# Kernel tuning notes

Hardware: AMD Instinct MI355X
Metric: run time of the kernel (lower is better)

The kernel has to match this reference:

```python
import jax, jax.numpy as jnp
import numpy as np
import math

EPS = 1.1920929e-07  # torch.finfo(float32).eps, used by nn.RMSNorm(eps=None)

def rmsnorm(x, w):
    return x * jax.lax.rsqrt(jnp.mean(x * x, axis=-1, keepdims=True) + EPS) * w

def sinkhorn(logits, iters=20):
    m = jnp.exp(logits - logits.max(axis=-1, keepdims=True))
    def body(_, m):
        m = m / (m.sum(axis=-1, keepdims=True) + 1e-6)
        return m / (m.sum(axis=-2, keepdims=True) + 1e-6)
    return jax.lax.fori_loop(0, iters, body, m)

def ngram_hash(ids, mults):
    # ids [B,T] int32, mults [2,2,3] int32 -> [B,T,4]
    B, T = ids.shape
    padded = jnp.pad(ids, ((0, 0), (2, 0)))
    windows = jnp.stack([padded[:, k:k + T] for k in range(3)], axis=-1)  # [B,T,3]
    out = []
    for n_idx in range(2):
        L = n_idx + 2
        grams = windows[:, :, 3 - L:]                                     # [B,T,L]
        mixed = grams[:, :, None, :] * mults[n_idx, :, :L][None, None]    # [B,T,2,L]
        h = mixed[..., 0]
        for k in range(1, L):
            h = jnp.bitwise_xor(h, mixed[..., k])
        out.append(h % 4096)
    return jnp.concatenate(out, axis=2)

def short_conv(x, conv_w, norm_w):
    # depthwise causal conv, kernel 4: torch pads 3 both sides then slices [..., :T]
    B, T, G, C = x.shape
    xn = rmsnorm(x, norm_w).reshape(B, T, G * C).transpose(0, 2, 1)  # [B,GC,T]
    y = jax.lax.conv_general_dilated(xn, conv_w, (1,), [(3, 0)],
                                     feature_group_count=G * C,
                                     dimension_numbers=('NCH', 'OIH', 'NCH'))
    return jax.nn.silu(y).transpose(0, 2, 1).reshape(B, T, G, C)

def engram(x, ids, mults, emb_table, val_w, val_b, key_w, key_b, nq_w, nk_w, conv_w, convnorm_w):
    B, T = ids.shape
    hash_ids = ngram_hash(ids, mults) + jnp.array([0, 4096, 8192, 12288], dtype=jnp.int32)
    emb = emb_table[hash_ids].reshape(B, T, -1)                       # [B,T,256]
    v_base = emb @ val_w + val_b                                      # [B,T,128]
    k = rmsnorm(jnp.einsum('btd,sdc->btsc', emb, key_w) + key_b, nk_w)  # [B,T,4,128]
    q = rmsnorm(x, nq_w)
    gates = jax.nn.sigmoid(jnp.sum(q * k, axis=-1, keepdims=True) / math.sqrt(128.0))
    v_gated = v_base[:, :, None, :] * gates                           # [B,T,4,128]
    return v_gated + short_conv(v_gated, conv_w, convnorm_w)

def causal_attn(x, qkv_w, qkv_b, proj_w, proj_b):
    B, T, C = x.shape
    H, D = 4, C // 4
    q, k, v = jnp.split(x @ qkv_w + qkv_b, 3, axis=-1)
    q = q.reshape(B, T, H, D).transpose(0, 2, 1, 3)
    k = k.reshape(B, T, H, D).transpose(0, 2, 1, 3)
    v = v.reshape(B, T, H, D).transpose(0, 2, 1, 3)
    att = jnp.einsum('bhtd,bhsd->bhts', q, k) / math.sqrt(D)
    att = jnp.where(jnp.tril(jnp.ones((T, T), bool)), att, -jnp.inf)
    att = jax.nn.softmax(att, axis=-1)
    y = jnp.einsum('bhts,bhsd->bhtd', att, v).transpose(0, 2, 1, 3).reshape(B, T, C)
    return y @ proj_w + proj_b

def mhc(x, layer_fn, coef_w, pre_w, pre_b, post_w, post_b, res_w, res_b, a_pre, a_post, a_res, ln_w):
    B, T, n, C = x.shape
    xn = rmsnorm(x.reshape(B * T, n * C), coef_w)
    H_pre = jax.nn.sigmoid(a_pre * (xn @ pre_w + pre_b))             # [BT,n]
    H_post = 2.0 * jax.nn.sigmoid(a_post * (xn @ post_w + post_b))   # [BT,n]
    H_res = sinkhorn((a_res * (xn @ res_w + res_b)).reshape(-1, n, n))
    xp = x.reshape(B * T, n, C)
    x_agg = jnp.einsum('bn,bnc->bc', H_pre, xp)
    y = layer_fn(rmsnorm(x_agg.reshape(B, T, C), ln_w)).reshape(B * T, C)
    # faithful to torch einsum 'bjn,bc->bnc' applied to H_post.transpose(1,2) [BT,n,1]:
    # the stream dim j is CONTRACTED, leaving a size-1 dim that broadcasts over streams
    x_branch = H_post.sum(axis=-1)[:, None, None] * y[:, None, :]    # [BT,1,C]
    x_highway = jnp.einsum('bnm,bmc->bnc', H_res, xp)                # [BT,n,C]
    return (x_highway + x_branch).reshape(B, T, n, C)

def _forward(x, input_ids, eng_multipliers, eng_embedding, eng_val_w, eng_val_b, eng_key_w, eng_key_b, eng_nq_w, eng_nk_w, eng_conv_w, eng_convnorm_w, a_coef_w, a_pre_w, a_pre_b, a_post_w, a_post_b, a_res_w, a_res_b, a_alpha_pre, a_alpha_post, a_alpha_res, a_ln_w, qkv_w, qkv_b, attnproj_w, attnproj_b, m_coef_w, m_pre_w, m_pre_b, m_post_w, m_post_b, m_res_w, m_res_b, m_alpha_pre, m_alpha_post, m_alpha_res, m_ln_w, mlp_w1, mlp_b1, mlp_w2, mlp_b2):
    x = x + engram(x, input_ids, eng_multipliers, eng_embedding, eng_val_w, eng_val_b, eng_key_w, eng_key_b, eng_nq_w, eng_nk_w, eng_conv_w, eng_convnorm_w)
    attn_fn = lambda z: causal_attn(z, qkv_w, qkv_b, attnproj_w, attnproj_b)
    x = mhc(x, attn_fn, a_coef_w, a_pre_w, a_pre_b, a_post_w, a_post_b, a_res_w, a_res_b, a_alpha_pre, a_alpha_post, a_alpha_res, a_ln_w)
    mlp_fn = lambda z: jax.nn.silu(z @ mlp_w1 + mlp_b1) @ mlp_w2 + mlp_b2
    x = mhc(x, mlp_fn, m_coef_w, m_pre_w, m_pre_b, m_post_w, m_post_b, m_res_w, m_res_b, m_alpha_pre, m_alpha_post, m_alpha_res, m_ln_w)
    return x

def setup_inputs():
    key = jax.random.key(0)
    B, T = 256, 128
    def rnd(i, shp, scale=0.02):
        return jax.random.normal(jax.random.fold_in(key, i), shp, jnp.float32) * scale
    alpha = jnp.asarray(0.01, jnp.float32)
    return {
        'x': rnd(0, (B, T, 4, 128), 1.0),
        'input_ids': jax.random.randint(jax.random.fold_in(key, 1), (B, T), 0, 4096, jnp.int32),
        'eng_multipliers': jax.random.randint(jax.random.fold_in(key, 2), (2, 2, 3), 1, 10000, jnp.int32),
        'eng_embedding': rnd(3, (16384, 64)),
        'eng_val_w': rnd(4, (256, 128)), 'eng_val_b': jnp.zeros(128, jnp.float32),
        'eng_key_w': rnd(5, (4, 256, 128)), 'eng_key_b': jnp.zeros((4, 128), jnp.float32),
        'eng_nq_w': jnp.ones((4, 128), jnp.float32), 'eng_nk_w': jnp.ones((4, 128), jnp.float32),
        'eng_conv_w': rnd(6, (512, 1, 4), 0.1), 'eng_convnorm_w': jnp.ones((4, 128), jnp.float32),
        'a_coef_w': jnp.ones(512, jnp.float32),
        'a_pre_w': rnd(7, (512, 4)), 'a_pre_b': jnp.zeros(4, jnp.float32),
        'a_post_w': rnd(8, (512, 4)), 'a_post_b': jnp.zeros(4, jnp.float32),
        'a_res_w': rnd(9, (512, 16)), 'a_res_b': jnp.zeros(16, jnp.float32),
        'a_alpha_pre': alpha, 'a_alpha_post': alpha, 'a_alpha_res': alpha,
        'a_ln_w': jnp.ones(128, jnp.float32),
        'qkv_w': rnd(10, (128, 384)), 'qkv_b': jnp.zeros(384, jnp.float32),
        'attnproj_w': rnd(11, (128, 128)), 'attnproj_b': jnp.zeros(128, jnp.float32),
        'm_coef_w': jnp.ones(512, jnp.float32),
        'm_pre_w': rnd(12, (512, 4)), 'm_pre_b': jnp.zeros(4, jnp.float32),
        'm_post_w': rnd(13, (512, 4)), 'm_post_b': jnp.zeros(4, jnp.float32),
        'm_res_w': rnd(14, (512, 16)), 'm_res_b': jnp.zeros(16, jnp.float32),
        'm_alpha_pre': alpha, 'm_alpha_post': alpha, 'm_alpha_res': alpha,
        'm_ln_w': jnp.ones(128, jnp.float32),
        'mlp_w1': rnd(15, (128, 512)), 'mlp_b1': jnp.zeros(512, jnp.float32),
        'mlp_w2': rnd(16, (512, 128)), 'mlp_b2': jnp.zeros(128, jnp.float32),
    }

def reference(x, input_ids, eng_multipliers, eng_embedding, eng_val_w, eng_val_b, eng_key_w, eng_key_b, eng_nq_w, eng_nk_w, eng_conv_w, eng_convnorm_w, a_coef_w, a_pre_w, a_pre_b, a_post_w, a_post_b, a_res_w, a_res_b, a_alpha_pre, a_alpha_post, a_alpha_res, a_ln_w, qkv_w, qkv_b, attnproj_w, attnproj_b, m_coef_w, m_pre_w, m_pre_b, m_post_w, m_post_b, m_res_w, m_res_b, m_alpha_pre, m_alpha_post, m_alpha_res, m_ln_w, mlp_w1, mlp_b1, mlp_w2, mlp_b2):
    return _forward(x, input_ids, eng_multipliers, eng_embedding, eng_val_w, eng_val_b, eng_key_w, eng_key_b, eng_nq_w, eng_nk_w, eng_conv_w, eng_convnorm_w, a_coef_w, a_pre_w, a_pre_b, a_post_w, a_post_b, a_res_w, a_res_b, a_alpha_pre, a_alpha_post, a_alpha_res, a_ln_w, qkv_w, qkv_b, attnproj_w, attnproj_b, m_coef_w, m_pre_w, m_pre_b, m_post_w, m_post_b, m_res_w, m_res_b, m_alpha_pre, m_alpha_post, m_alpha_res, m_ln_w, mlp_w1, mlp_b1, mlp_w2, mlp_b2)
```

## Files before the change

### kernel.cpp

```cpp
#include <hip/hip_runtime.h>

#define BT 32768
#define TSEQ 128

constexpr float EPSF = 1.1920929e-07f;

typedef __attribute__((ext_vector_type(8))) short bf16x8;
typedef __attribute__((ext_vector_type(4))) float f32x4;

__device__ __forceinline__ float sigm(float z) { return 1.f / (1.f + __expf(-z)); }

__device__ __forceinline__ short bf16c(float f) {
  union { float f; unsigned u; } v; v.f = f;
  unsigned r = v.u + 0x7FFFu + ((v.u >> 16) & 1u);
  return (short)(r >> 16);
}
__device__ __forceinline__ float bf2f(short s) {
  union { unsigned u; float f; } v; v.u = ((unsigned)(unsigned short)s) << 16;
  return v.f;
}

__device__ __forceinline__ float red64(float v) {
  v += __shfl_xor(v, 1);  v += __shfl_xor(v, 2);  v += __shfl_xor(v, 4);
  v += __shfl_xor(v, 8);  v += __shfl_xor(v, 16); v += __shfl_xor(v, 32);
  return v;
}
__device__ __forceinline__ float red32(float v) {
  v += __shfl_xor(v, 1); v += __shfl_xor(v, 2); v += __shfl_xor(v, 4);
  v += __shfl_xor(v, 8); v += __shfl_xor(v, 16);
  return v;
}
__device__ __forceinline__ float red16(float v) {
  v += __shfl_xor(v, 1); v += __shfl_xor(v, 2); v += __shfl_xor(v, 4); v += __shfl_xor(v, 8);
  return v;
}
__device__ __forceinline__ float redmax16(float v) {
  v = fmaxf(v, __shfl_xor(v, 1)); v = fmaxf(v, __shfl_xor(v, 2));
  v = fmaxf(v, __shfl_xor(v, 4)); v = fmaxf(v, __shfl_xor(v, 8));
  return v;
}
__device__ __forceinline__ void load8(float* d, const float* p) {
  const float4 a = *reinterpret_cast<const float4*>(p);
  const float4 b = *reinterpret_cast<const float4*>(p + 4);
  d[0]=a.x; d[1]=a.y; d[2]=a.z; d[3]=a.w; d[4]=b.x; d[5]=b.y; d[6]=b.z; d[7]=b.w;
}

__global__ __launch_bounds__(256) void prep(
    const float* __restrict__ qkv_w, const float* __restrict__ proj_w,
    const float* __restrict__ mlp_w1, const float* __restrict__ mlp_w2,
    const float* __restrict__ val_w, const float* __restrict__ key_w,
    const float* __restrict__ a_res_w, const float* __restrict__ a_pre_w,
    const float* __restrict__ a_post_w,
    const float* __restrict__ m_res_w, const float* __restrict__ m_pre_w,
    const float* __restrict__ m_post_w,
    const float* __restrict__ a_res_b, const float* __restrict__ a_pre_b,
    const float* __restrict__ a_post_b,
    const float* __restrict__ m_res_b, const float* __restrict__ m_pre_b,
    const float* __restrict__ m_post_b,
    short* __restrict__ wt_qkv, short* __restrict__ wt_proj,
    short* __restrict__ wt_mlp1, short* __restrict__ wt_mlp2,
    short* __restrict__ wt_eng, short* __restrict__ wpk_a,
    short* __restrict__ wpk_m, float* __restrict__ bpk_a,
    float* __restrict__ bpk_m)
{
  const int idx = blockIdx.x * 256 + threadIdx.x;
  if (idx < 49152) {
    const int n = idx >> 7, k = idx & 127;
    wt_qkv[idx] = bf16c(qkv_w[k * 384 + n]);
  } else if (idx < 65536) {
    const int j = idx - 49152; const int n = j >> 7, k = j & 127;
    wt_proj[j] = bf16c(proj_w[k * 128 + n]);
  } else if (idx < 131072) {
    const int j = idx - 65536; const int n = j >> 7, k = j & 127;
    wt_mlp1[j] = bf16c(mlp_w1[k * 512 + n]);
  } else if (idx < 196608) {
    const int j = idx - 131072; const int n = j >> 9, k = j & 511;
    wt_mlp2[j] = bf16c(mlp_w2[k * 128 + n]);
  } else if (idx < 360448) {
    const int j = idx - 196608; const int n = j >> 8, k = j & 255;
    float v;
    if (n < 128) v = val_w[k * 128 + n];
    else v = key_w[(size_t)((n - 128) >> 7) * 32768 + k * 128 + (n & 127)];
    wt_eng[j] = bf16c(v);
  } else if (idx < 376832) {
    const int j = idx - 360448; const int r = j >> 9, k = j & 511;
    float v = 0.f;
    if (r < 16) v = a_res_w[k * 16 + r];
    else if (r < 20) v = a_pre_w[k * 4 + (r - 16)];
    else if (r < 24) v = a_post_w[k * 4 + (r - 20)];
    wpk_a[j] = bf16c(v);
  } else if (idx < 393216) {
    const int j = idx - 376832; const int r = j >> 9, k = j & 511;
    float v = 0.f;
    if (r < 16) v = m_res_w[k * 16 + r];
    else if (r < 20) v = m_pre_w[k * 4 + (r - 16)];
    else if (r < 24) v = m_post_w[k * 4 + (r - 20)];
    wpk_m[j] = bf16c(v);
  } else if (idx < 393280) {
    const int j = idx - 393216;
    if (j < 32) {
      float v = 0.f;
      if (j < 16) v = a_res_b[j];
      else if (j < 20) v = a_pre_b[j - 16];
      else if (j < 24) v = a_post_b[j - 20];
      bpk_a[j] = v;
    } else {
      const int r = j - 32;
      float v = 0.f;
      if (r < 16) v = m_res_b[r];
      else if (r < 20) v = m_pre_b[r - 16];
      else if (r < 24) v = m_post_b[r - 20];
      bpk_m[r] = v;
    }
  }
}

__global__ __launch_bounds__(256) void mgemm32(
    const float* __restrict__ A, const int lda,
    const short* __restrict__ WT, const float* __restrict__ bias,
    float* __restrict__ out, const int K,
    const float* __restrict__ rinv, const float* __restrict__ csc)
{
  __shared__ short As[64 * 64];
  __shared__ short Bs[32 * 64];
  const int tid = threadIdx.x;
  const int i0 = blockIdx.x * 64;
  const int w = tid >> 6, l = tid & 63;
  const int wm = w >> 1, wn = w & 1;
  const int kg = l >> 4, lr = l & 15;
  f32x4 acc[2];
  acc[0] = {0.f, 0.f, 0.f, 0.f};
  acc[1] = {0.f, 0.f, 0.f, 0.f};

  const int c4 = tid & 15;
  const int asl = c4 >> 1, ahf = c4 & 1;

  for (int kc = 0; kc < K; kc += 64) {
    __syncthreads();
#pragma unroll
    for (int p = 0; p < 4; ++p) {
      const int r = (tid >> 4) + p * 16;
      float4 v = *reinterpret_cast<const float4*>(A + (size_t)(i0 + r) * lda + kc + c4 * 4);
      const float rs = rinv[i0 + r];
      const float4 cs = *reinterpret_cast<const float4*>(csc + kc + c4 * 4);
      v.x *= rs * cs.x; v.y *= rs * cs.y; v.z *= rs * cs.z; v.w *= rs * cs.w;
      short4 b4; b4.x = bf16c(v.x); b4.y = bf16c(v.y); b4.z = bf16c(v.z); b4.w = bf16c(v.w);
      *reinterpret_cast<short4*>(&As[r * 64 + ((asl ^ (r & 7)) << 3) + (ahf << 2)]) = b4;
    }
    {
      const int r = tid >> 3, slb = tid & 7;
      const bf16x8 v = *reinterpret_cast<const bf16x8*>(WT + (size_t)r * K + kc + slb * 8);
      *reinterpret_cast<bf16x8*>(&Bs[r * 64 + ((slb ^ (r & 7)) << 3)]) = v;
    }
    __syncthreads();
#pragma unroll
    for (int ks = 0; ks < 2; ++ks) {
      const int slot = ks * 4 + kg;
      bf16x8 af[2], bft;
#pragma unroll
      for (int mi = 0; mi < 2; ++mi) {
        const int r = wm * 32 + mi * 16 + lr;
        af[mi] = *reinterpret_cast<const bf16x8*>(&As[r * 64 + ((slot ^ (r & 7)) << 3)]);
      }
      {
        const int rb = wn * 16 + lr;
        bft = *reinterpret_cast<const bf16x8*>(&Bs[rb * 64 + ((slot ^ (rb & 7)) << 3)]);
      }
#pragma unroll
      for (int mi = 0; mi < 2; ++mi)
        acc[mi] = __builtin_amdgcn_mfma_f32_16x16x32_bf16(af[mi], bft, acc[mi], 0, 0, 0);
    }
  }
#pragma unroll
  for (int mi = 0; mi < 2; ++mi) {
    const int col = wn * 16 + lr;
    const float bv = bias[col];
#pragma unroll
    for (int j = 0; j < 4; ++j) {
      const int row = i0 + wm * 32 + mi * 16 + kg * 4 + j;
      out[(size_t)row * 32 + col] = acc[mi][j] + bv;
    }
  }
}

__global__ __launch_bounds__(256) void eng_mgemm(
    const int* __restrict__ ids, const int* __restrict__ mults,
    const float* __restrict__ table, const float* __restrict__ val_b,
    const short* __restrict__ wt_eng,
    float* __restrict__ vbase, unsigned short* __restrict__ krawb)
{
  __shared__ int hid[128][4];
  __shared__ short As[128 * 64];
  __shared__ short Bs[128 * 64];
  const int tid = threadIdx.x;
  const int i0 = blockIdx.x * 128;
  const int by = blockIdx.y;
  const int c0 = by * 128;
#pragma unroll
  for (int p = 0; p < 2; ++p) {
    const int idx = tid + p * 256;
    const int r = idx >> 2, wh = idx & 3;
    const int i = i0 + r;
    const int b = i >> 7, tt = i & 127;
    const int* __restrict__ row = ids + b * TSEQ;
    const int g2 = row[tt];
    const int g1 = (tt >= 1) ? row[tt - 1] : 0;
    const int g0 = (tt >= 2) ? row[tt - 2] : 0;
    int h;
    if (wh == 0)      h = ((g1 * mults[0]) ^ (g2 * mults[1])) & 4095;
    else if (wh == 1) h = (((g1 * mults[3]) ^ (g2 * mults[4])) & 4095) + 4096;
    else if (wh == 2) h = (((g0 * mults[6]) ^ (g1 * mults[7]) ^ (g2 * mults[8])) & 4095) + 8192;
    else              h = (((g0 * mults[9]) ^ (g1 * mults[10]) ^ (g2 * mults[11])) & 4095) + 12288;
    hid[r][wh] = h;
  }
  const int w = tid >> 6, l = tid & 63;
  const int wr = (w >> 1) * 64, wc = (w & 1) * 64;
  f32x4 acc[4][4];
#pragma unroll
  for (int mi = 0; mi < 4; ++mi)
#pragma unroll
    for (int ni = 0; ni < 4; ++ni) acc[mi][ni] = {0.f, 0.f, 0.f, 0.f};

  const int c4 = tid & 15;
  const int asl = c4 >> 1, ahf = c4 & 1;
  const int bsl = tid & 7;

  for (int kc = 0; kc < 256; kc += 64) {
    const int seg = kc >> 6;
    __syncthreads();
#pragma unroll
    for (int p = 0; p < 8; ++p) {
      const int r = (tid >> 4) + p * 16;
      const float4 v = *reinterpret_cast<const float4*>(table + (size_t)hid[r][seg] * 64 + c4 * 4);
      short4 b4; b4.x = bf16c(v.x); b4.y = bf16c(v.y); b4.z = bf16c(v.z); b4.w = bf16c(v.w);
      *reinterpret_cast<short4*>(&As[r * 64 + ((asl ^ (r & 7)) << 3) + (ahf << 2)]) = b4;
    }
#pragma unroll
    for (int p = 0; p < 4; ++p) {
      const int r = (tid >> 3) + p * 32;
      const bf16x8 v = *reinterpret_cast<const bf16x8*>(wt_eng + (size_t)(c0 + r) * 256 + kc + bsl * 8);
      *reinterpret_cast<bf16x8*>(&Bs[r * 64 + ((bsl ^ (r & 7)) << 3)]) = v;
    }
    __syncthreads();
    const int kg = l >> 4, lr = l & 15;
#pragma unroll
    for (int ks = 0; ks < 2; ++ks) {
      const int slot = ks * 4 + kg;
      bf16x8 af[4], bft[4];
#pragma unroll
      for (int mi = 0; mi < 4; ++mi) {
        const int r = wr + mi * 16 + lr;
        af[mi] = *reinterpret_cast<const bf16x8*>(&As[r * 64 + ((slot ^ (r & 7)) << 3)]);
      }
#pragma unroll
      for (int ni = 0; ni < 4; ++ni) {
        const int r = wc + ni * 16 + lr;
        bft[ni] = *reinterpret_cast<const bf16x8*>(&Bs[r * 64 + ((slot ^ (r & 7)) << 3)]);
      }
#pragma unroll
      for (int mi = 0; mi < 4; ++mi)
#pragma unroll
        for (int ni = 0; ni < 4; ++ni)
          acc[mi][ni] = __builtin_amdgcn_mfma_f32_16x16x32_bf16(af[mi], bft[ni], acc[mi][ni], 0, 0, 0);
    }
  }
  const int lr = l & 15, hi = l >> 4;
#pragma unroll
  for (int mi = 0; mi < 4; ++mi)
#pragma unroll
    for (int ni = 0; ni < 4; ++ni) {
      const int col = wc + ni * 16 + lr;
#pragma unroll
      for (int j = 0; j < 4; ++j) {
        const int row = i0 + wr + mi * 16 + hi * 4 + j;
        if (by == 0)
          vbase[(size_t)row * 128 + col] = acc[mi][ni][j] + val_b[col];
        else
          krawb[(size_t)row * 512 + (by - 1) * 128 + col] =
              (unsigned short)bf16c(acc[mi][ni][j]);
      }
    }
}

__global__ __launch_bounds__(256) void fused_gateconv(
    const unsigned short* __restrict__ krawb, const float* __restrict__ x,
    const float* __restrict__ vbase, const float* __restrict__ key_b,
    const float* __restrict__ nk_w, const float* __restrict__ nq_w,
    const float* __restrict__ conv_w, const float* __restrict__ cnw,
    float* __restrict__ xout, float* __restrict__ invout)
{
  __shared__ float vb[19 * 128];
  __shared__ float gA[19][4];
  __shared__ float gG[19][4];
  const int tid = threadIdx.x;
  const size_t rowbase = (size_t)blockIdx.x * 16;
  const int tt0 = (int)(rowbase & 127);
#pragma unroll
  for (int p = 0; p < 3; ++p) {
    const int idx = p * 256 + tid;
    if (idx < 608) {
      const int hs = idx >> 5, c4 = (idx & 31) << 2;
      float4 v = make_float4(0.f, 0.f, 0.f, 0.f);
      if (tt0 - 3 + hs >= 0)
        v = *reinterpret_cast<const float4*>(vbase + (rowbase - 3 + hs) * 128 + c4);
      *reinterpret_cast<float4*>(&vb[hs * 128 + c4]) = v;
    }
  }
  __syncthreads();
  const int w = tid >> 6, l = tid & 63;
  {
    const int s = l >> 4, li = l & 15, c0 = li * 8, j0 = l * 8;
    float kb[8], nk[8], nq[8];
    load8(kb, key_b + s * 128 + c0);
    load8(nk, nk_w + s * 128 + c0);
    load8(nq, nq_w + s * 128 + c0);
    for (int it = 0; it < 5; ++it) {
      const int ht = it * 4 + w;
      if (ht >= 19) break;
      const int tt = tt0 - 3 + ht;
      if (tt < 0) {
        if (li == 0) { gG[ht][s] = 0.f; gA[ht][s] = 0.f; }
        continue;
      }
      const size_t rg = rowbase - 3 + ht;
      float kv[8], xv[8];
      {
        const bf16x8 kvb = *reinterpret_cast<const bf16x8*>(krawb + rg * 512 + j0);
#pragma unroll
        for (int jj = 0; jj < 8; ++jj) kv[jj] = bf2f(kvb[jj]);
      }
      load8(xv, x + rg * 512 + j0);
      float ssk = 0.f, ssx = 0.f;
#pragma unroll
      for (int jj = 0; jj < 8; ++jj) {
        kv[jj] += kb[jj];
        ssk = fmaf(kv[jj], kv[jj], ssk);
        ssx = fmaf(xv[jj], xv[jj], ssx);
      }
      ssk = red16(ssk);
      ssx = red16(ssx);
      const float invk = rsqrtf(ssk * (1.f / 128.f) + EPSF);
      const float invq = rsqrtf(ssx * (1.f / 128.f) + EPSF);
      float dot = 0.f;
#pragma unroll
      for (int jj = 0; jj < 8; ++jj)
        dot = fmaf(kv[jj] * invk * nk[jj], xv[jj] * invq * nq[jj], dot);
      dot = red16(dot);
      const float gate = sigm(dot * 0.08838834764831843f);
      const float2 vb2 = *reinterpret_cast<const float2*>(&vb[ht * 128 + l * 2]);
      float ssv = vb2.x * vb2.x + vb2.y * vb2.y;
      ssv = red64(ssv);
      const float A = gate * rsqrtf(gate * gate * (ssv * (1.f / 128.f)) + EPSF);
      if (li == 0) { gG[ht][s] = gate; gA[ht][s] = A; }
    }
  }
  __syncthreads();
  {
    const int tg = tid >> 5;
    const int c4l = tid & 31;
    const int cf = c4l * 4;
    for (int ti = 0; ti < 2; ++ti) {
      const int t = tg + ti * 8;
      const size_t rg = rowbase + t;
      float ssq = 0.f;
#pragma unroll
      for (int sj = 0; sj < 4; ++sj) {
        const int j = sj * 128 + cf;
        float4 cwe[4];
#pragma unroll
        for (int e = 0; e < 4; ++e)
          cwe[e] = *reinterpret_cast<const float4*>(conv_w + (size_t)(j + e) * 4);
        const float4 cn4 = *reinterpret_cast<const float4*>(cnw + j);
        float4 vbt[4]; float av[4];
#pragma unroll
        for (int kk = 0; kk < 4; ++kk) {
          vbt[kk] = *reinterpret_cast<const float4*>(&vb[(t + kk) * 128 + cf]);
          av[kk] = gA[t + kk][sj];
        }
        const float gg = gG[t + 3][sj];
        float4 accv;
        accv.x = vbt[0].x*av[0]*cwe[0].x + vbt[1].x*av[1]*cwe[0].y + vbt[2].x*av[2]*cwe[0].z + vbt[3].x*av[3]*cwe[0].w;
        accv.y = vbt[0].y*av[0]*cwe[1].x + vbt[1].y*av[1]*cwe[1].y + vbt[2].y*av[2]*cwe[1].z + vbt[3].y*av[3]*cwe[1].w;
        accv.z = vbt[0].z*av[0]*cwe[2].x + vbt[1].z*av[1]*cwe[2].y + vbt[2].z*av[2]*cwe[2].z + vbt[3].z*av[3]*cwe[2].w;
        accv.w = vbt[0].w*av[0]*cwe[3].x + vbt[1].w*av[1]*cwe[3].y + vbt[2].w*av[2]*cwe[3].z + vbt[3].w*av[3]*cwe[3].w;
        const float4 x4 = *reinterpret_cast<const float4*>(x + rg * 512 + j);
        const float y0 = accv.x * cn4.x, y1 = accv.y * cn4.y;
        const float y2 = accv.z * cn4.z, y3 = accv.w * cn4.w;
        float4 o;
        o.x = x4.x + vbt[3].x * gg + y0 * sigm(y0);
        o.y = x4.y + vbt[3].y * gg + y1 * sigm(y1);
        o.z = x4.z + vbt[3].z * gg + y2 * sigm(y2);
        o.w = x4.w + vbt[3].w * gg + y3 * sigm(y3);
        *reinterpret_cast<float4*>(xout + rg * 512 + j) = o;
        ssq += o.x*o.x + o.y*o.y + o.z*o.z + o.w*o.w;
      }
      ssq = red32(ssq);
      if (c4l == 0) invout[rg] = rsqrtf(ssq * (1.f / 512.f) + EPSF);
    }
  }
}

__global__ __launch_bounds__(256) void mhc_sink2(
    const float* __restrict__ proj, const float* __restrict__ xin,
    const float* __restrict__ p_apre, const float* __restrict__ p_apost,
    const float* __restrict__ p_ares, const float* __restrict__ ln_w,
    unsigned short* __restrict__ xab, float* __restrict__ hres,
    float* __restrict__ hps)
{
  const int tid = threadIdx.x;
  const int l = tid & 63;
  const size_t i = (size_t)blockIdx.x * 4 + (tid >> 6);
  const float pv = proj[i * 32 + (l & 31)];
  const float apre = p_apre[0], apost = p_apost[0], ares = p_ares[0];
  const int n = l >> 4;
  const float hp = sigm(apre * __shfl(pv, 16 + n));
  float hsum = 0.f;
#pragma unroll
  for (int t2 = 0; t2 < 4; ++t2) hsum += 2.f * sigm(apost * __shfl(pv, 20 + t2));
  const float v = ares * pv;
  float rm = fmaxf(v, __shfl_xor(v, 1));
  rm = fmaxf(rm, __shfl_xor(rm, 2));
  float m = __expf(v - rm);
#pragma unroll
  for (int it = 0; it < 20; ++it) {
    float rs = m + __shfl_xor(m, 1);
    rs += __shfl_xor(rs, 2);
    m *= __builtin_amdgcn_rcpf(rs + 1e-6f);
    float cs = m + __shfl_xor(m, 4);
    cs += __shfl_xor(cs, 8);
    m *= __builtin_amdgcn_rcpf(cs + 1e-6f);
  }
  if (l < 16) hres[i * 16 + l] = m;
  if (l == 0) hps[i] = hsum;
  const int j0 = l * 8;
  float xv[8];
  load8(xv, xin + i * 512 + j0);
  float ag[8];
#pragma unroll
  for (int jj = 0; jj < 8; ++jj) {
    float a2 = hp * xv[jj];
    a2 += __shfl_xor(a2, 16);
    a2 += __shfl_xor(a2, 32);
    ag[jj] = a2;
  }
  float ssa = 0.f;
#pragma unroll
  for (int jj = 0; jj < 8; ++jj) ssa = fmaf(ag[jj], ag[jj], ssa);
  ssa = red16(ssa);
  const float inva = rsqrtf(ssa * (1.f / 128.f) + EPSF);
  if (l < 16) {
    float lnw[8];
    load8(lnw, ln_w + l * 8);
    bf16x8 o;
#pragma unroll
    for (int jj = 0; jj < 8; ++jj) o[jj] = bf16c(ag[jj] * inva * lnw[jj]);
    *reinterpret_cast<bf16x8*>(xab + i * 128 + l * 8) = o;
  }
}

template <int NT, int ACT>
__global__ __launch_bounds__(256) void mgemm_bf16A(
    const unsigned short* __restrict__ Ab, const short* __restrict__ WT,
    const float* __restrict__ bias, unsigned short* __restrict__ outp)
{
  __shared__ short As[128 * 64];
  __shared__ short Bs[128 * 64];
  const int tid = threadIdx.x;
  const int i0 = blockIdx.x * 128;
  const int c0 = blockIdx.y * 128;
  const int w = tid >> 6, l = tid & 63;
  const int wr = (w >> 1) * 64, wc = (w & 1) * 64;
  const int kg = l >> 4, lr = l & 15;
  f32x4 acc[4][4];
#pragma unroll
  for (int mi = 0; mi < 4; ++mi)
#pragma unroll
    for (int ni = 0; ni < 4; ++ni) acc[mi][ni] = {0.f, 0.f, 0.f, 0.f};

#pragma unroll
  for (int kc = 0; kc < 2; ++kc) {
    __syncthreads();
#pragma unroll
    for (int p = 0; p < 4; ++p) {
      const int idx = p * 256 + tid;
      const int r = idx >> 3, slb = idx & 7;
      const bf16x8 v = *reinterpret_cast<const bf16x8*>(Ab + (size_t)(i0 + r) * 128 + kc * 64 + slb * 8);
      *reinterpret_cast<bf16x8*>(&As[r * 64 + ((slb ^ (r & 7)) << 3)]) = v;
    }
#pragma unroll
    for (int p = 0; p < 4; ++p) {
      const int idx = p * 256 + tid;
      const int r = idx >> 3, slb = idx & 7;
      const bf16x8 v = *reinterpret_cast<const bf16x8*>(WT + (size_t)(c0 + r) * 128 + kc * 64 + slb * 8);
      *reinterpret_cast<bf16x8*>(&Bs[r * 64 + ((slb ^ (r & 7)) << 3)]) = v;
    }
    __syncthreads();
#pragma unroll
    for (int ks = 0; ks < 2; ++ks) {
      const int slot = ks * 4 + kg;
      bf16x8 af[4], bft[4];
#pragma unroll
      for (int mi = 0; mi < 4; ++mi) {
        const int r = wr + mi * 16 + lr;
        af[mi] = *reinterpret_cast<const bf16x8*>(&As[r * 64 + ((slot ^ (r & 7)) << 3)]);
      }
#pragma unroll
      for (int ni = 0; ni < 4; ++ni) {
        const int r = wc + ni * 16 + lr;
        bft[ni] = *reinterpret_cast<const bf16x8*>(&Bs[r * 64 + ((slot ^ (r & 7)) << 3)]);
      }
#pragma unroll
      for (int mi = 0; mi < 4; ++mi)
#pragma unroll
        for (int ni = 0; ni < 4; ++ni)
          acc[mi][ni] = __builtin_amdgcn_mfma_f32_16x16x32_bf16(af[mi], bft[ni], acc[mi][ni], 0, 0, 0);
    }
  }
#pragma unroll
  for (int mi = 0; mi < 4; ++mi)
#pragma unroll
    for (int ni = 0; ni < 4; ++ni) {
      const int col = c0 + wc + ni * 16 + lr;
      const float bv = bias[col];
#pragma unroll
      for (int j = 0; j < 4; ++j) {
        const int row = i0 + wr + mi * 16 + kg * 4 + j;
        float o = acc[mi][ni][j] + bv;
        if (ACT == 1) o = o * sigm(o);
        outp[(size_t)row * (NT * 128) + col] = (unsigned short)bf16c(o);
      }
    }
}

template <int KT, bool WITH_INV>
__global__ __launch_bounds__(512) void gemm_combine(
    const unsigned short* __restrict__ Ab, const int lda,
    const short* __restrict__ WT, const float* __restrict__ bias,
    const float* __restrict__ xst, const float* __restrict__ hres,
    const float* __restrict__ hps, float* __restrict__ outp,
    float* __restrict__ invout)
{
  __shared__ short As[64 * 64];
  __shared__ short Bs[128 * 64];
  __shared__ short yl[64 * 132];
  __shared__ float prt[64][2];
  const int tid = threadIdx.x;
  const size_t i0 = (size_t)blockIdx.x * 64;
  const int w = tid >> 6, l = tid & 63;
  const int wm = w >> 2, wn = w & 3;
  const int kg = l >> 4, lr = l & 15;
  f32x4 acc[2][2];
#pragma unroll
  for (int mi = 0; mi < 2; ++mi)
#pragma unroll
    for (int ni = 0; ni < 2; ++ni) acc[mi][ni] = {0.f, 0.f, 0.f, 0.f};
#pragma unroll
  for (int kc = 0; kc < KT; ++kc) {
    __syncthreads();
    {
      const int r = tid >> 3, slb = tid & 7;
      const bf16x8 v = *reinterpret_cast<const bf16x8*>(Ab + (i0 + r) * lda + kc * 64 + slb * 8);
      *reinterpret_cast<bf16x8*>(&As[r * 64 + ((slb ^ (r & 7)) << 3)]) = v;
    }
#pragma unroll
    for (int p = 0; p < 2; ++p) {
      const int idx = p * 512 + tid;
      const int r = idx >> 3, slb = idx & 7;
      const bf16x8 v = *reinterpret_cast<const bf16x8*>(
          WT + (size_t)r * (KT * 64) + kc * 64 + slb * 8);
      *reinterpret_cast<bf16x8*>(&Bs[r * 64 + ((slb ^ (r & 7)) << 3)]) = v;
    }
    __syncthreads();
#pragma unroll
    for (int ks = 0; ks < 2; ++ks) {
      const int slot = ks * 4 + kg;
      bf16x8 af[2], bft[2];
#pragma unroll
      for (int mi = 0; mi < 2; ++mi) {
        const int r = wm * 32 + mi * 16 + lr;
        af[mi] = *reinterpret_cast<const bf16x8*>(&As[r * 64 + ((slot ^ (r & 7)) << 3)]);
      }
#pragma unroll
      for (int ni = 0; ni < 2; ++ni) {
        const int rb = wn * 32 + ni * 16 + lr;
        bft[ni] = *reinterpret_cast<const bf16x8*>(&Bs[rb * 64 + ((slot ^ (rb & 7)) << 3)]);
      }
#pragma unroll
      for (int mi = 0; mi < 2; ++mi)
#pragma unroll
        for (int ni = 0; ni < 2; ++ni)
          acc[mi][ni] = __builtin_amdgcn_mfma_f32_16x16x32_bf16(af[mi], bft[ni], acc[mi][ni], 0, 0, 0);
    }
  }
#pragma unroll
  for (int mi = 0; mi < 2; ++mi)
#pragma unroll
    for (int ni = 0; ni < 2; ++ni) {
      const int col = wn * 32 + ni * 16 + lr;
      const float bv = bias[col];
#pragma unroll
      for (int j = 0; j < 4; ++j) {
        const int row = wm * 32 + mi * 16 + kg * 4 + j;
        yl[row * 132 + col] = bf16c(acc[mi][ni][j] + bv);
      }
    }
  __syncthreads();
  const int c = tid & 127, tl = tid >> 7;
  for (int k = 0; k < 16; ++k) {
    const int t = tl * 16 + k;
    const size_t rg = i0 + t;
    float hv[16];
#pragma unroll
    for (int n16 = 0; n16 < 16; ++n16) hv[n16] = hres[rg * 16 + n16];
    const float g = hps[rg];
    const float yv = bf2f(yl[t * 132 + c]) * g;
    float xm[4];
#pragma unroll
    for (int m = 0; m < 4; ++m) xm[m] = xst[rg * 512 + m * 128 + c];
    float ssq = 0.f;
#pragma unroll
    for (int n = 0; n < 4; ++n) {
      const float o = hv[n*4+0]*xm[0] + hv[n*4+1]*xm[1] + hv[n*4+2]*xm[2] + hv[n*4+3]*xm[3] + yv;
      outp[rg * 512 + n * 128 + c] = o;
      if (WITH_INV) ssq = fmaf(o, o, ssq);
    }
    if (WITH_INV) {
      ssq = red64(ssq);
      if (l == 0) prt[t][(tid >> 6) & 1] = ssq;
    }
  }
  if (WITH_INV) {
    __syncthreads();
    if (tid < 64)
      invout[i0 + tid] = rsqrtf((prt[tid][0] + prt[tid][1]) * (1.f / 512.f) + EPSF);
  }
}

__global__ __launch_bounds__(256) void attn_mfma(
    const unsigned short* __restrict__ qkv, unsigned short* __restrict__ y)
{
  __shared__ short Ks[128 * 32];
  __shared__ short Vt[32 * 128];
  __shared__ short Ps[4][32 * 128];
  const int tid = threadIdx.x;
  const int b = blockIdx.x >> 2, h = blockIdx.x & 3;
  const unsigned short* __restrict__ base = qkv + (size_t)b * 128 * 384 + h * 32;
#pragma unroll
  for (int p = 0; p < 2; ++p) {
    const int idx = tid + p * 256;
    const int s = idx >> 2, c8 = idx & 3;
    const bf16x8 v = *reinterpret_cast<const bf16x8*>(base + (size_t)s * 384 + 128 + c8 * 8);
    const int chunk = c8 ^ ((s >> 1) & 3);
    *reinterpret_cast<bf16x8*>(&Ks[s * 32 + chunk * 8]) = v;
  }
#pragma unroll
  for (int p = 0; p < 4; ++p) {
    const int idx = tid + p * 256;
    const int s = idx >> 3, c4 = idx & 7;
    const ushort4 v = *reinterpret_cast<const ushort4*>(base + (size_t)s * 384 + 256 + c4 * 4);
    const int schunk = s >> 3, soff = s & 7;
#pragma unroll
    for (int k = 0; k < 4; ++k) {
      const int d = c4 * 4 + k;
      const unsigned short vv = (k == 0) ? v.x : (k == 1) ? v.y : (k == 2) ? v.z : v.w;
      Vt[d * 128 + ((schunk ^ (d & 7)) << 3) + soff] = (short)vv;
    }
  }
  const int w = tid >> 6, l = tid & 63;
  const int g = l >> 4, lr = l & 15;
  bf16x8 qa[2];
#pragma unroll
  for (int mi = 0; mi < 2; ++mi) {
    const int row = w * 32 + mi * 16 + lr;
    qa[mi] = *reinterpret_cast<const bf16x8*>(base + (size_t)row * 384 + g * 8);
  }
  __syncthreads();
  const int ntmax = 2 * w + 1;
  bf16x8 ka[8];
#pragma unroll
  for (int nt = 0; nt < 8; ++nt)
    if (nt <= ntmax) {
      const int s = nt * 16 + lr;
      const int chunk = g ^ ((s >> 1) & 3);
      ka[nt] = *reinterpret_cast<const bf16x8*>(&Ks[s * 32 + chunk * 8]);
    }
  f32x4 sacc[2][8];
#pragma unroll
  for (int mi = 0; mi < 2; ++mi)
#pragma unroll
    for (int nt = 0; nt < 8; ++nt) sacc[mi][nt] = {0.f, 0.f, 0.f, 0.f};
#pragma unroll
  for (int mi = 0; mi < 2; ++mi)
#pragma unroll
    for (int nt = 0; nt < 8; ++nt)
      if (nt <= ntmax)
        sacc[mi][nt] = __builtin_amdgcn_mfma_f32_16x16x32_bf16(qa[mi], ka[nt], sacc[mi][nt], 0, 0, 0);
  const float scl = 0.17677669529663687f;
  float rv[2][4];
  short* const pw = Ps[w];
#pragma unroll
  for (int mi = 0; mi < 2; ++mi) {
#pragma unroll
    for (int j = 0; j < 4; ++j) {
      const int row = w * 32 + mi * 16 + g * 4 + j;
      float mx = -3.4e38f;
#pragma unroll
      for (int nt = 0; nt < 8; ++nt)
        if (nt <= ntmax) {
          const int col = nt * 16 + lr;
          const float val = sacc[mi][nt][j] * scl;
          if (col <= row) mx = fmaxf(mx, val);
        }
      mx = redmax16(mx);
      float sum = 0.f;
      const int rl = mi * 16 + g * 4 + j;
#pragma unroll
      for (int nt = 0; nt < 8; ++nt)
        if (nt <= ntmax) {
          const int col = nt * 16 + lr;
          const float val = sacc[mi][nt][j] * scl;
          const float pv = (col <= row) ? __expf(val - mx) : 0.f;
          sum += pv;
          const int chunk = (2 * nt + (lr >> 3)) ^ (rl & 7);
          pw[rl * 128 + chunk * 8 + (lr & 7)] = bf16c(pv);
        }
      sum = red16(sum);
      rv[mi][j] = 1.f / sum;
    }
  }
  f32x4 oacc[2][2];
#pragma unroll
  for (int mi = 0; mi < 2; ++mi)
#pragma unroll
    for (int nt = 0; nt < 2; ++nt) oacc[mi][nt] = {0.f, 0.f, 0.f, 0.f};
#pragma unroll
  for (int kt = 0; kt < 4; ++kt)
    if (kt <= w) {
      bf16x8 pa[2], va[2];
#pragma unroll
      for (int mi = 0; mi < 2; ++mi) {
        const int rl = mi * 16 + lr;
        const int chunk = (4 * kt + g) ^ (rl & 7);
        pa[mi] = *reinterpret_cast<const bf16x8*>(&pw[rl * 128 + chunk * 8]);
      }
#pragma unroll
      for (int nt = 0; nt < 2; ++nt) {
        const int d = nt * 16 + lr;
        const int chunk = (4 * kt + g) ^ (d & 7);
        va[nt] = *reinterpret_cast<const bf16x8*>(&Vt[d * 128 + chunk * 8]);
      }
#pragma unroll
      for (int mi = 0; mi < 2; ++mi)
#pragma unroll
        for (int nt = 0; nt < 2; ++nt)
          oacc[mi][nt] = __builtin_amdgcn_mfma_f32_16x16x32_bf16(pa[mi], va[nt], oacc[mi][nt], 0, 0, 0);
    }
#pragma unroll
  for (int mi = 0; mi < 2; ++mi)
#pragma unroll
    for (int nt = 0; nt < 2; ++nt)
#pragma unroll
      for (int j = 0; j < 4; ++j) {
        const int row = w * 32 + mi * 16 + g * 4 + j;
        y[((size_t)b * 128 + row) * 128 + h * 32 + nt * 16 + lr] =
            (unsigned short)bf16c(oacc[mi][nt][j] * rv[mi][j]);
      }
}

extern "C" void kernel_launch(void* const* d_in, const int* in_sizes, int n_in,
                              void* d_out, int out_size, void* d_ws, size_t ws_size,
                              hipStream_t stream)
{
  const float* x        = (const float*)d_in[0];
  const int*   ids      = (const int*)d_in[1];
  const int*   mults    = (const int*)d_in[2];
  const float* table    = (const float*)d_in[3];
  const float* val_w    = (const float*)d_in[4];
  const float* val_b    = (const float*)d_in[5];
  const float* key_w    = (const float*)d_in[6];
  const float* key_b    = (const float*)d_in[7];
  const float* nq_w     = (const float*)d_in[8];
  const float* nk_w     = (const float*)d_in[9];
  const float* conv_w   = (const float*)d_in[10];
  const float* cnw      = (const float*)d_in[11];
  const float* a_coef   = (const float*)d_in[12];
  const float* a_pre_w  = (const float*)d_in[13];
  const float* a_pre_b  = (const float*)d_in[14];
  const float* a_post_w = (const float*)d_in[15];
  const float* a_post_b = (const float*)d_in[16];
  const float* a_res_w  = (const float*)d_in[17];
  const float* a_res_b  = (const float*)d_in[18];
  const float* a_apre   = (const float*)d_in[19];
  const float* a_apost  = (const float*)d_in[20];
  const float* a_ares   = (const float*)d_in[21];
  const float* a_ln_w   = (const float*)d_in[22];
  const float* qkv_w    = (const float*)d_in[23];
  const float* qkv_b    = (const float*)d_in[24];
  const float* proj_w   = (const float*)d_in[25];
  const float* proj_b   = (const float*)d_in[26];
  const float* m_coef   = (const float*)d_in[27];
  const float* m_pre_w  = (const float*)d_in[28];
  const float* m_pre_b  = (const float*)d_in[29];
  const float* m_post_w = (const float*)d_in[30];
  const float* m_post_b = (const float*)d_in[31];
  const float* m_res_w  = (const float*)d_in[32];
  const float* m_res_b  = (const float*)d_in[33];
  const float* m_apre   = (const float*)d_in[34];
  const float* m_apost  = (const float*)d_in[35];
  const float* m_ares   = (const float*)d_in[36];
  const float* m_ln_w   = (const float*)d_in[37];
  const float* mlp_w1   = (const float*)d_in[38];
  const float* mlp_b1   = (const float*)d_in[39];
  const float* mlp_w2   = (const float*)d_in[40];
  const float* mlp_b2   = (const float*)d_in[41];

  float* out = (float*)d_out;
  float* ws  = (float*)d_ws;
  float* x2     = ws;
  float* vbase  = ws;
  float* proj24 = x2 + (size_t)BT * 512;
  float* hresb  = proj24 + (size_t)BT * 32;
  float* hpsb   = hresb + (size_t)BT * 16;
  float* inv1   = hpsb + (size_t)BT;
  float* inv2   = inv1 + (size_t)BT;
  float* bpk_a  = inv2 + (size_t)BT;
  float* bpk_m  = bpk_a + 32;
  short* wt_qkv  = (short*)(bpk_m + 32);
  short* wt_proj = wt_qkv  + 49152;
  short* wt_mlp1 = wt_proj + 16384;
  short* wt_mlp2 = wt_mlp1 + 65536;
  short* wt_eng  = wt_mlp2 + 65536;
  short* wpk_a   = wt_eng  + 163840;
  short* wpk_m   = wpk_a   + 16384;
  unsigned short* xab = (unsigned short*)(wpk_m + 16384);
  unsigned short* big = xab + (size_t)BT * 128;
  unsigned short* y1b = big + (size_t)BT * 512;

  prep<<<1537, 256, 0, stream>>>(qkv_w, proj_w, mlp_w1, mlp_w2, val_w, key_w,
                                 a_res_w, a_pre_w, a_post_w, m_res_w, m_pre_w, m_post_w,
                                 a_res_b, a_pre_b, a_post_b, m_res_b, m_pre_b, m_post_b,
                                 wt_qkv, wt_proj, wt_mlp1, wt_mlp2, wt_eng,
                                 wpk_a, wpk_m, bpk_a, bpk_m);

  eng_mgemm<<<dim3(BT / 128, 5), 256, 0, stream>>>(ids, mults, table, val_b, wt_eng,
                                                   vbase, big);
  fused_gateconv<<<BT / 16, 256, 0, stream>>>(big, x, vbase, key_b, nk_w, nq_w,
                                              conv_w, cnw, out, inv1);

  mgemm32<<<BT / 64, 256, 0, stream>>>(out, 512, wpk_a, bpk_a, proj24, 512, inv1, a_coef);
  mhc_sink2<<<BT / 4, 256, 0, stream>>>(proj24, out, a_apre, a_apost, a_ares, a_ln_w,
                                        xab, hresb, hpsb);
  mgemm_bf16A<3, 0><<<dim3(BT / 128, 3), 256, 0, stream>>>(xab, wt_qkv, qkv_b, big);
  attn_mfma<<<1024, 256, 0, stream>>>(big, y1b);
  gemm_combine<2, true><<<BT / 64, 512, 0, stream>>>(y1b, 128, wt_proj, proj_b,
                                                     out, hresb, hpsb, x2, inv2);

  mgemm32<<<BT / 64, 256, 0, stream>>>(x2, 512, wpk_m, bpk_m, proj24, 512, inv2, m_coef);
  mhc_sink2<<<BT / 4, 256, 0, stream>>>(proj24, x2, m_apre, m_apost, m_ares, m_ln_w,
                                        xab, hresb, hpsb);
  mgemm_bf16A<4, 1><<<dim3(BT / 128, 4), 256, 0, stream>>>(xab, wt_mlp1, mlp_b1, big);
  gemm_combine<8, false><<<BT / 64, 512, 0, stream>>>(big, 512, wt_mlp2, mlp_b2,
                                                      x2, hresb, hpsb, out, nullptr);

  (void)in_sizes; (void)n_in; (void)out_size; (void)ws_size;
}
```

Measured before the change: 300.7 us.

## Store intermediate residual streams in bf16 instead of fp32

The residual streams x1 (after engram) and x2 (after attention) are now written and read as bf16 rather than fp32. This roughly halves the HBM traffic of the consumers: mgemm32, mhc_sink2 and gemm_combine. The rms inverse is still computed from fp32 values before rounding. The cost is reduced precision in the residual path that feeds the final output, plus a workspace layout change that aliases y1b onto xab.

```diff
diff --git a/kernel.cpp b/kernel.cpp
--- a/kernel.cpp
+++ b/kernel.cpp
@@ -116,7 +116,7 @@
 }
 
 __global__ __launch_bounds__(256) void mgemm32(
-    const float* __restrict__ A, const int lda,
+    const unsigned short* __restrict__ Ab, const int lda,
     const short* __restrict__ WT, const float* __restrict__ bias,
     float* __restrict__ out, const int K,
     const float* __restrict__ rinv, const float* __restrict__ csc)
@@ -132,20 +132,26 @@
   acc[0] = {0.f, 0.f, 0.f, 0.f};
   acc[1] = {0.f, 0.f, 0.f, 0.f};
 
-  const int c4 = tid & 15;
-  const int asl = c4 >> 1, ahf = c4 & 1;
-
   for (int kc = 0; kc < K; kc += 64) {
     __syncthreads();
 #pragma unroll
-    for (int p = 0; p < 4; ++p) {
-      const int r = (tid >> 4) + p * 16;
-      float4 v = *reinterpret_cast<const float4*>(A + (size_t)(i0 + r) * lda + kc + c4 * 4);
+    for (int p = 0; p < 2; ++p) {
+      const int idx = p * 256 + tid;
+      const int r = idx >> 3, ko = idx & 7;
+      const bf16x8 v = *reinterpret_cast<const bf16x8*>(Ab + (size_t)(i0 + r) * lda + kc + ko * 8);
       const float rs = rinv[i0 + r];
-      const float4 cs = *reinterpret_cast<const float4*>(csc + kc + c4 * 4);
-      v.x *= rs * cs.x; v.y *= rs * cs.y; v.z *= rs * cs.z; v.w *= rs * cs.w;
-      short4 b4; b4.x = bf16c(v.x); b4.y = bf16c(v.y); b4.z = bf16c(v.z); b4.w = bf16c(v.w);
-      *reinterpret_cast<short4*>(&As[r * 64 + ((asl ^ (r & 7)) << 3) + (ahf << 2)]) = b4;
+      const float4 ca = *reinterpret_cast<const float4*>(csc + kc + ko * 8);
+      const float4 cb = *reinterpret_cast<const float4*>(csc + kc + ko * 8 + 4);
+      bf16x8 o;
+      o[0] = bf16c(bf2f(v[0]) * rs * ca.x);
+      o[1] = bf16c(bf2f(v[1]) * rs * ca.y);
+      o[2] = bf16c(bf2f(v[2]) * rs * ca.z);
+      o[3] = bf16c(bf2f(v[3]) * rs * ca.w);
+      o[4] = bf16c(bf2f(v[4]) * rs * cb.x);
+      o[5] = bf16c(bf2f(v[5]) * rs * cb.y);
+      o[6] = bf16c(bf2f(v[6]) * rs * cb.z);
+      o[7] = bf16c(bf2f(v[7]) * rs * cb.w);
+      *reinterpret_cast<bf16x8*>(&As[r * 64 + ((ko ^ (r & 7)) << 3)]) = o;
     }
     {
       const int r = tid >> 3, slb = tid & 7;
@@ -287,7 +293,7 @@
     const float* __restrict__ vbase, const float* __restrict__ key_b,
     const float* __restrict__ nk_w, const float* __restrict__ nq_w,
     const float* __restrict__ conv_w, const float* __restrict__ cnw,
-    float* __restrict__ xout, float* __restrict__ invout)
+    unsigned short* __restrict__ xout, float* __restrict__ invout)
 {
   __shared__ float vb[19 * 128];
   __shared__ float gA[19][4];
@@ -391,7 +397,12 @@
         o.y = x4.y + vbt[3].y * gg + y1 * sigm(y1);
         o.z = x4.z + vbt[3].z * gg + y2 * sigm(y2);
         o.w = x4.w + vbt[3].w * gg + y3 * sigm(y3);
-        *reinterpret_cast<float4*>(xout + rg * 512 + j) = o;
+        ushort4 ob;
+        ob.x = (unsigned short)bf16c(o.x);
+        ob.y = (unsigned short)bf16c(o.y);
+        ob.z = (unsigned short)bf16c(o.z);
+        ob.w = (unsigned short)bf16c(o.w);
+        *reinterpret_cast<ushort4*>(xout + rg * 512 + j) = ob;
         ssq += o.x*o.x + o.y*o.y + o.z*o.z + o.w*o.w;
       }
       ssq = red32(ssq);
@@ -401,7 +412,7 @@
 }
 
 __global__ __launch_bounds__(256) void mhc_sink2(
-    const float* __restrict__ proj, const float* __restrict__ xin,
+    const float* __restrict__ proj, const unsigned short* __restrict__ xin,
     const float* __restrict__ p_apre, const float* __restrict__ p_apost,
     const float* __restrict__ p_ares, const float* __restrict__ ln_w,
     unsigned short* __restrict__ xab, float* __restrict__ hres,
@@ -434,7 +445,11 @@
   if (l == 0) hps[i] = hsum;
   const int j0 = l * 8;
   float xv[8];
-  load8(xv, xin + i * 512 + j0);
+  {
+    const bf16x8 xb = *reinterpret_cast<const bf16x8*>(xin + i * 512 + j0);
+#pragma unroll
+    for (int jj = 0; jj < 8; ++jj) xv[jj] = bf2f(xb[jj]);
+  }
   float ag[8];
 #pragma unroll
   for (int jj = 0; jj < 8; ++jj) {
@@ -532,12 +547,12 @@
     }
 }
 
-template <int KT, bool WITH_INV>
+template <int KT, bool WITH_INV, bool OUTBF>
 __global__ __launch_bounds__(512) void gemm_combine(
     const unsigned short* __restrict__ Ab, const int lda,
     const short* __restrict__ WT, const float* __restrict__ bias,
-    const float* __restrict__ xst, const float* __restrict__ hres,
-    const float* __restrict__ hps, float* __restrict__ outp,
+    const unsigned short* __restrict__ xst, const float* __restrict__ hres,
+    const float* __restrict__ hps, void* __restrict__ outp,
     float* __restrict__ invout)
 {
   __shared__ short As[64 * 64];
@@ -616,12 +631,15 @@
     const float yv = bf2f(yl[t * 132 + c]) * g;
     float xm[4];
 #pragma unroll
-    for (int m = 0; m < 4; ++m) xm[m] = xst[rg * 512 + m * 128 + c];
+    for (int m = 0; m < 4; ++m) xm[m] = bf2f((short)xst[rg * 512 + m * 128 + c]);
     float ssq = 0.f;
 #pragma unroll
     for (int n = 0; n < 4; ++n) {
       const float o = hv[n*4+0]*xm[0] + hv[n*4+1]*xm[1] + hv[n*4+2]*xm[2] + hv[n*4+3]*xm[3] + yv;
-      outp[rg * 512 + n * 128 + c] = o;
+      if (OUTBF)
+        ((unsigned short*)outp)[rg * 512 + n * 128 + c] = (unsigned short)bf16c(o);
+      else
+        ((float*)outp)[rg * 512 + n * 128 + c] = o;
       if (WITH_INV) ssq = fmaf(o, o, ssq);
     }
     if (WITH_INV) {
@@ -816,9 +834,8 @@
 
   float* out = (float*)d_out;
   float* ws  = (float*)d_ws;
-  float* x2     = ws;
   float* vbase  = ws;
-  float* proj24 = x2 + (size_t)BT * 512;
+  float* proj24 = vbase + (size_t)BT * 128;
   float* hresb  = proj24 + (size_t)BT * 32;
   float* hpsb   = hresb + (size_t)BT * 16;
   float* inv1   = hpsb + (size_t)BT;
@@ -834,7 +851,9 @@
   short* wpk_m   = wpk_a   + 16384;
   unsigned short* xab = (unsigned short*)(wpk_m + 16384);
   unsigned short* big = xab + (size_t)BT * 128;
-  unsigned short* y1b = big + (size_t)BT * 512;
+  unsigned short* x1b = big + (size_t)BT * 512;
+  unsigned short* x2b = x1b + (size_t)BT * 512;
+  unsigned short* y1b = xab;
 
   prep<<<1537, 256, 0, stream>>>(qkv_w, proj_w, mlp_w1, mlp_w2, val_w, key_w,
                                  a_res_w, a_pre_w, a_post_w, m_res_w, m_pre_w, m_post_w,
@@ -845,22 +864,22 @@
   eng_mgemm<<<dim3(BT / 128, 5), 256, 0, stream>>>(ids, mults, table, val_b, wt_eng,
                                                    vbase, big);
   fused_gateconv<<<BT / 16, 256, 0, stream>>>(big, x, vbase, key_b, nk_w, nq_w,
-                                              conv_w, cnw, out, inv1);
-
-  mgemm32<<<BT / 64, 256, 0, stream>>>(out, 512, wpk_a, bpk_a, proj24, 512, inv1, a_coef);
-  mhc_sink2<<<BT / 4, 256, 0, stream>>>(proj24, out, a_apre, a_apost, a_ares, a_ln_w,
+                                              conv_w, cnw, x1b, inv1);
+
+  mgemm32<<<BT / 64, 256, 0, stream>>>(x1b, 512, wpk_a, bpk_a, proj24, 512, inv1, a_coef);
+  mhc_sink2<<<BT / 4, 256, 0, stream>>>(proj24, x1b, a_apre, a_apost, a_ares, a_ln_w,
                                         xab, hresb, hpsb);
   mgemm_bf16A<3, 0><<<dim3(BT / 128, 3), 256, 0, stream>>>(xab, wt_qkv, qkv_b, big);
   attn_mfma<<<1024, 256, 0, stream>>>(big, y1b);
-  gemm_combine<2, true><<<BT / 64, 512, 0, stream>>>(y1b, 128, wt_proj, proj_b,
-                                                     out, hresb, hpsb, x2, inv2);
-
-  mgemm32<<<BT / 64, 256, 0, stream>>>(x2, 512, wpk_m, bpk_m, proj24, 512, inv2, m_coef);
-  mhc_sink2<<<BT / 4, 256, 0, stream>>>(proj24, x2, m_apre, m_apost, m_ares, m_ln_w,
+  gemm_combine<2, true, true><<<BT / 64, 512, 0, stream>>>(
+      y1b, 128, wt_proj, proj_b, x1b, hresb, hpsb, (void*)x2b, inv2);
+
+  mgemm32<<<BT / 64, 256, 0, stream>>>(x2b, 512, wpk_m, bpk_m, proj24, 512, inv2, m_coef);
+  mhc_sink2<<<BT / 4, 256, 0, stream>>>(proj24, x2b, m_apre, m_apost, m_ares, m_ln_w,
                                         xab, hresb, hpsb);
   mgemm_bf16A<4, 1><<<dim3(BT / 128, 4), 256, 0, stream>>>(xab, wt_mlp1, mlp_b1, big);
-  gemm_combine<8, false><<<BT / 64, 512, 0, stream>>>(big, 512, wt_mlp2, mlp_b2,
-                                                      x2, hresb, hpsb, out, nullptr);
+  gemm_combine<8, false, false><<<BT / 64, 512, 0, stream>>>(
+      big, 512, wt_mlp2, mlp_b2, x2b, hresb, hpsb, (void*)out, nullptr);
 
   (void)in_sizes; (void)n_in; (void)out_size; (void)ws_size;
 }
```

Measured after the change: 290.8 us. -3.3%, faster.
